# Kernel optimization log

Hardware: AMD Instinct MI355X
Metric: run time of the kernel (lower is better)

The kernel has to match this reference:

```python
import jax, jax.numpy as jnp
import numpy as np

B, N, C, T = 512, 62, 8, 64
K = 8          # topk
HEADS = 4
OUT = 128
EPS = 1e-5     # BatchNorm1d eps
NEG_SLOPE = 0.2  # GATConv leaky_relu slope


def _gat(x, W, a_src, a_dst, bias, src, dst, valid, num_nodes, concat):
    """PyG GATConv (eval mode, self-loops already in edge list)."""
    H, Co = a_src.shape[1], a_src.shape[2]
    xl = (x @ W.T).reshape(num_nodes, H, Co)          # [V,H,Co]
    al_src = jnp.sum(xl * a_src, axis=-1)             # [V,H]
    al_dst = jnp.sum(xl * a_dst, axis=-1)             # [V,H]
    alpha = jax.nn.leaky_relu(al_src[src] + al_dst[dst], NEG_SLOPE)  # [E,H]
    alpha = jnp.where(valid[:, None], alpha, -jnp.inf)
    amax = jax.ops.segment_max(alpha, dst, num_segments=num_nodes)   # [V,H]
    ex = jnp.where(valid[:, None], jnp.exp(alpha - amax[dst]), 0.0)
    denom = jax.ops.segment_sum(ex, dst, num_segments=num_nodes)     # [V,H]
    w = ex / denom[dst]                                              # softmax per dst
    out = jax.ops.segment_sum(xl[src] * w[:, :, None], dst, num_segments=num_nodes)
    out = out.reshape(num_nodes, H * Co) if concat else out.mean(axis=1)
    return out + bias


def reference(x, edge_index, W1, W2, b_sp, V_sp, bn_w, bn_b,
              g1_w, g1_asrc, g1_adst, g1_b, g2_w, g2_asrc, g2_adst, g2_b):
    # edge_index is unused: spatial=True rebuilds the graph from attention.
    x4 = x.reshape(B, N, C, T)
    # SpatialAttention: ((x @ W1) @ W2) -> tanh(. @ V + b) -> BatchNorm1d(N)
    prod = jnp.einsum('bnct,t->bnc', x4, W1) @ W2      # [B,N,N]
    S = jnp.tanh(prod @ V_sp + b_sp)                   # [B,N,N]
    mean = S.mean(axis=(0, 2), keepdims=True)          # BN over channel dim 1
    var = S.var(axis=(0, 2), keepdims=True)
    adj = (S - mean) / jnp.sqrt(var + EPS) * bn_w[None, :, None] + bn_b[None, :, None]
    # topk mask + dense_to_sparse: exactly K edges per (batch, row)
    _, idx = jax.lax.top_k(adj, K)                     # [B,N,K] column indices
    offs = (jnp.arange(B) * N)[:, None, None]
    src = (jnp.broadcast_to(jnp.arange(N)[None, :, None], (B, N, K)) + offs).reshape(-1)
    dst = (idx + offs).reshape(-1)
    # GATConv: remove_self_loops then add_self_loops -> mask topk self-edges, append loops
    loops = jnp.arange(B * N)
    valid = jnp.concatenate([src != dst, jnp.ones(B * N, dtype=bool)])
    src = jnp.concatenate([src, loops])
    dst = jnp.concatenate([dst, loops])
    h = x4.reshape(B * N, C * T)
    h = jax.nn.relu(_gat(h, g1_w, g1_asrc, g1_adst, g1_b, src, dst, valid, B * N, True))
    h = jax.nn.relu(_gat(h, g2_w, g2_asrc, g2_adst, g2_b, src, dst, valid, B * N, False))
    return h


def setup_inputs() -> dict:
    key = jax.random.key(0)
    ks = jax.random.split(key, 16)
    d_in = C * T  # 512
    return {
        'x': jax.random.normal(ks[0], (B, N, C, T), jnp.float32),
        'edge_index': jax.random.randint(ks[1], (2, 128), 0, B * N, jnp.int64) if False else jax.random.randint(ks[1], (2, 128), 0, B * N).astype(jnp.int32),
        'W1': jax.random.uniform(ks[2], (T,), jnp.float32),
        'W2': jax.random.normal(ks[3], (C, N), jnp.float32) * 0.1,
        'b_sp': jax.random.normal(ks[4], (1, N, N), jnp.float32) * 0.1,
        'V_sp': jax.random.normal(ks[5], (N, N), jnp.float32) * 0.1,
        'bn_w': jnp.ones((N,), jnp.float32),
        'bn_b': jnp.zeros((N,), jnp.float32),
        'g1_w': jax.random.normal(ks[6], (HEADS * OUT, d_in), jnp.float32) * 0.04,
        'g1_asrc': jax.random.normal(ks[7], (1, HEADS, OUT), jnp.float32) * 0.06,
        'g1_adst': jax.random.normal(ks[8], (1, HEADS, OUT), jnp.float32) * 0.06,
        'g1_b': jnp.zeros((HEADS * OUT,), jnp.float32),
        'g2_w': jax.random.normal(ks[9], (HEADS * OUT, HEADS * OUT), jnp.float32) * 0.04,
        'g2_asrc': jax.random.normal(ks[10], (1, HEADS, OUT), jnp.float32) * 0.06,
        'g2_adst': jax.random.normal(ks[11], (1, HEADS, OUT), jnp.float32) * 0.06,
        'g2_b': jnp.zeros((OUT,), jnp.float32),
    }
```

## Files before the change

### kernel.cpp

```cpp
#include <hip/hip_runtime.h>
#include <math.h>

#define B_ 512
#define N_ 62
#define V_ (B_ * N_)
#define MP_ (B_ * 64)
#define TOPK_ 8

typedef __attribute__((ext_vector_type(8))) short bf16x8;
typedef __attribute__((ext_vector_type(4))) float f32x4;

__device__ __forceinline__ unsigned short bf16rn(float f) {
    unsigned int u = __float_as_uint(f);
    unsigned int r = (u + 0x7fffu + ((u >> 16) & 1u)) >> 16;
    return (unsigned short)r;
}
__device__ __forceinline__ float bf16tof(unsigned short h) {
    return __uint_as_float(((unsigned int)h) << 16);
}

__device__ __forceinline__ void gload16(const void* g, void* l) {
    __builtin_amdgcn_global_load_lds(
        (const __attribute__((address_space(1))) unsigned int*)g,
        (__attribute__((address_space(3))) unsigned int*)l, 16, 0, 0);
}

__global__ __launch_bounds__(256) void spatial_S(
    const float* __restrict__ x, const float* __restrict__ W1,
    const float* __restrict__ W2, const float* __restrict__ bsp,
    const float* __restrict__ Vsp, float* __restrict__ S,
    unsigned short* __restrict__ A2)
{
    int w = threadIdx.x >> 6, lane = threadIdx.x & 63;
    int blk = blockIdx.x * 4 + w;
    int b = blk / N_, n = blk - b * N_;
    const float* xr = x + (size_t)blk * 512;
    float w1 = W1[lane];

    float y[8];
#pragma unroll
    for (int c = 0; c < 8; ++c) {
        float xv = xr[c * 64 + lane];
        A2[((size_t)(b * 64 + n)) * 512 + c * 64 + lane] = bf16rn(xv);
        float p = xv * w1;
#pragma unroll
        for (int off = 32; off; off >>= 1) p += __shfl_xor(p, off);
        y[c] = p;
    }

    __shared__ float pr[4][N_];
    if (lane < N_) {
        float acc = 0.f;
#pragma unroll
        for (int c = 0; c < 8; ++c) acc += y[c] * W2[c * N_ + lane];
        pr[w][lane] = acc;
    }
    __syncthreads();
    if (lane < N_) {
        float acc = bsp[n * N_ + lane];
        for (int k = 0; k < N_; ++k) acc += pr[w][k] * Vsp[k * N_ + lane];
        S[(size_t)blk * N_ + lane] = tanhf(acc);
    }
}

__global__ __launch_bounds__(256) void bn_part(
    const float* __restrict__ S, double* __restrict__ part)
{
    int n = blockIdx.x >> 4, slice = blockIdx.x & 15;
    double s = 0.0, s2 = 0.0;
    int i0 = slice * 1984;
    for (int i = i0 + threadIdx.x; i < i0 + 1984; i += 256) {
        int b = i / N_, m = i - b * N_;
        float v = S[((size_t)b * N_ + n) * N_ + m];
        s += v; s2 += (double)v * v;
    }
    __shared__ double sh[256], sh2[256];
    sh[threadIdx.x] = s; sh2[threadIdx.x] = s2;
    __syncthreads();
    for (int off = 128; off; off >>= 1) {
        if (threadIdx.x < off) {
            sh[threadIdx.x] += sh[threadIdx.x + off];
            sh2[threadIdx.x] += sh2[threadIdx.x + off];
        }
        __syncthreads();
    }
    if (threadIdx.x == 0) {
        part[((size_t)n * 16 + slice) * 2 + 0] = sh[0];
        part[((size_t)n * 16 + slice) * 2 + 1] = sh2[0];
    }
}

__global__ __launch_bounds__(64) void bn_final(
    const double* __restrict__ part, const float* __restrict__ bnw,
    const float* __restrict__ bnb, float* __restrict__ scale,
    float* __restrict__ shift)
{
    int n = threadIdx.x;
    if (n >= N_) return;
    double s = 0.0, s2 = 0.0;
    for (int j = 0; j < 16; ++j) {
        s  += part[((size_t)n * 16 + j) * 2 + 0];
        s2 += part[((size_t)n * 16 + j) * 2 + 1];
    }
    const double cnt = (double)(B_ * N_);
    double mean = s / cnt;
    double var = s2 / cnt - mean * mean;
    float inv = (float)(1.0 / sqrt(var + 1e-5));
    scale[n] = bnw[n] * inv;
    shift[n] = bnb[n] - (float)mean * bnw[n] * inv;
}

__global__ __launch_bounds__(64) void topk_mask(
    const float* __restrict__ S, const float* __restrict__ scale,
    const float* __restrict__ shift, unsigned long long* __restrict__ maskT)
{
    int blk = blockIdx.x;
    int b = blk / N_, n = blk - b * N_;
    int lane = threadIdx.x;
    float v = (lane < N_) ? S[(size_t)blk * N_ + lane] * scale[n] + shift[n]
                          : -INFINITY;
    bool sel = false;
#pragma unroll
    for (int k = 0; k < TOPK_; ++k) {
        float mv = v; int mi = lane;
#pragma unroll
        for (int off = 32; off; off >>= 1) {
            float ov = __shfl_xor(mv, off);
            int   oi = __shfl_xor(mi, off);
            if (ov > mv || (ov == mv && oi < mi)) { mv = ov; mi = oi; }
        }
        if (lane == mi) { sel = true; v = -INFINITY; }
    }
    unsigned long long row = __ballot(sel) | (1ull << n);
    if (lane < N_ && ((row >> lane) & 1ull))
        atomicOr(&maskT[(size_t)b * N_ + lane], 1ull << n);
}

__global__ __launch_bounds__(256) void zero_u64(unsigned long long* p, int n)
{
    int i = blockIdx.x * 256 + threadIdx.x;
    if (i < n) p[i] = 0ull;
}

__global__ __launch_bounds__(256) void split_pair(
    const float* __restrict__ in, unsigned short* __restrict__ out, int total4)
{
    int gid = blockIdx.x * 256 + threadIdx.x;
    if (gid >= total4) return;
    int row = gid >> 7;
    int c = (gid & 127) * 4;
    float4 v = ((const float4*)in)[gid];
    ushort4 h, l;
    float f;
    h.x = bf16rn(v.x); f = v.x - bf16tof(h.x); l.x = bf16rn(f);
    h.y = bf16rn(v.y); f = v.y - bf16tof(h.y); l.y = bf16rn(f);
    h.z = bf16rn(v.z); f = v.z - bf16tof(h.z); l.z = bf16rn(f);
    h.w = bf16rn(v.w); f = v.w - bf16tof(h.w); l.w = bf16rn(f);
    *(ushort4*)(&out[(size_t)row * 1024 + c])       = h;
    *(ushort4*)(&out[(size_t)row * 1024 + 512 + c]) = l;
}

__global__ __launch_bounds__(256) void gemm_bf16(
    const unsigned short* __restrict__ Ah, const unsigned short* __restrict__ Bw,
    unsigned short* __restrict__ XT,
    const float* __restrict__ asrc, const float* __restrict__ adst,
    float* __restrict__ als, float* __restrict__ ald)
{
    __shared__ __align__(16) unsigned short smem[16384];
    char* As = (char*)smem;
    char* Bs = (char*)(smem + 8192);

    int tid = threadIdx.x;
    int lane = tid & 63, w = tid >> 6;

    int flat = blockIdx.y * 4 + blockIdx.x;
    int swz = (flat & 7) * 128 + (flat >> 3);
    int by = swz >> 2, bx = swz & 3;
    int bm = by * 128, bn = bx * 128;

    int wr = w >> 1, wc = w & 1;

    f32x4 acc[4][4];
#pragma unroll
    for (int mf = 0; mf < 4; ++mf)
#pragma unroll
        for (int nf = 0; nf < 4; ++nf) acc[mf][nf] = (f32x4){0.f, 0.f, 0.f, 0.f};

    int srow = w * 8 + (lane >> 3);
    int kcol = (lane & 7) ^ (lane >> 3);
    int ldsoff = w * 1024;

    for (int kt = 0; kt < 16; ++kt) {
        int k0 = (kt & 7) * 64;
        int bBase = (kt >> 3) * 512 + k0;
#pragma unroll
        for (int i = 0; i < 4; ++i) {
            int row = i * 32 + srow;
            gload16(Ah + (size_t)(bm + row) * 512 + k0 + kcol * 8,
                    As + i * 4096 + ldsoff);
            gload16(Bw + (size_t)(bn + row) * 1024 + bBase + kcol * 8,
                    Bs + i * 4096 + ldsoff);
        }
        __syncthreads();

#pragma unroll
        for (int kk = 0; kk < 2; ++kk) {
            bf16x8 af[4], bfr[4];
#pragma unroll
            for (int mf = 0; mf < 4; ++mf)
                af[mf] = *(const bf16x8*)(As + (wr*64 + mf*16 + (lane&15))*128
                                             + ((kk*4 + (lane>>4)) ^ (lane&7))*16);
#pragma unroll
            for (int nf = 0; nf < 4; ++nf)
                bfr[nf] = *(const bf16x8*)(Bs + (wc*64 + nf*16 + (lane&15))*128
                                              + ((kk*4 + (lane>>4)) ^ (lane&7))*16);
#pragma unroll
            for (int mf = 0; mf < 4; ++mf)
#pragma unroll
                for (int nf = 0; nf < 4; ++nf)
                    acc[mf][nf] = __builtin_amdgcn_mfma_f32_16x16x32_bf16(
                        af[mf], bfr[nf], acc[mf][nf], 0, 0, 0);
        }
        __syncthreads();
    }

    int cc = lane & 15, lh = lane >> 4;
    int bb = (bm >> 6) + wr;
    int c0 = bn + wc * 64 + cc;
    int hH = bn >> 7;
    float as4[4], ad4[4];
#pragma unroll
    for (int nf = 0; nf < 4; ++nf) {
        as4[nf] = asrc[c0 + nf * 16];
        ad4[nf] = adst[c0 + nf * 16];
    }

#pragma unroll
    for (int mf = 0; mf < 4; ++mf) {
        int s = lh * 4 + mf * 16;
        f32x4 ts = (f32x4){0.f, 0.f, 0.f, 0.f};
        f32x4 td = (f32x4){0.f, 0.f, 0.f, 0.f};
#pragma unroll
        for (int nf = 0; nf < 4; ++nf) {
            ushort4 hv, lv;
#pragma unroll
            for (int r = 0; r < 4; ++r) {
                float v = acc[mf][nf][r];
                unsigned short hb = bf16rn(v);
                ((unsigned short*)&hv)[r] = hb;
                ((unsigned short*)&lv)[r] = bf16rn(v - bf16tof(hb));
                ts[r] += v * as4[nf];
                td[r] += v * ad4[nf];
            }
            size_t cb = ((size_t)bb * 1024 + c0 + nf * 16) * 64 + s;
            *(ushort4*)(XT + cb) = hv;
            *(ushort4*)(XT + cb + (size_t)512 * 64) = lv;
        }
#pragma unroll
        for (int off = 1; off < 16; off <<= 1) {
#pragma unroll
            for (int r = 0; r < 4; ++r) {
                ts[r] += __shfl_xor(ts[r], off);
                td[r] += __shfl_xor(td[r], off);
            }
        }
        if (cc == 0) {
#pragma unroll
            for (int r = 0; r < 4; ++r) {
                atomicAdd(&als[((size_t)bb * 64 + s + r) * 4 + hH], ts[r]);
                atomicAdd(&ald[((size_t)bb * 64 + s + r) * 4 + hH], td[r]);
            }
        }
    }
}

template <int APPLY>
__global__ __launch_bounds__(512, 8) void gat_aggM(
    const unsigned short* __restrict__ XT,
    const float* __restrict__ als, const float* __restrict__ ald,
    const unsigned long long* __restrict__ maskT,
    const float* __restrict__ bias,
    void* __restrict__ outp)
{
    __shared__ __align__(16) char lds[34816];
    float* shs = (float*)(lds + 32768);
    float* shd = (float*)(lds + 33792);

    int b = blockIdx.x;
    int tid = threadIdx.x;
    int lane = tid & 63, w = tid >> 6;

    if (tid < 256) {
        shs[tid] = als[(size_t)b * 256 + tid];
        shd[tid] = ald[(size_t)b * 256 + tid];
    }
    __syncthreads();

    for (int t = w; t < 248; t += 8) {
        int d = t >> 2, h = t & 3;
        unsigned long long m = maskT[(size_t)b * N_ + d];
        bool valid = (lane < N_) && ((m >> lane) & 1ull);
        float a = -INFINITY;
        if (valid) {
            float raw = shs[lane * 4 + h] + shd[d * 4 + h];
            a = (raw > 0.f) ? raw : 0.2f * raw;
        }
        float mx = a;
#pragma unroll
        for (int off = 32; off; off >>= 1) mx = fmaxf(mx, __shfl_xor(mx, off));
        float ex = valid ? expf(a - mx) : 0.f;
        float sm = ex;
#pragma unroll
        for (int off = 32; off; off >>= 1) sm += __shfl_xor(sm, off);
        float wv = valid ? ex / sm : 0.f;
        int addr = h * 8192 + d * 128
                 + (((lane >> 3) ^ (d & 7)) << 4) + ((lane & 7) << 1);
        *(unsigned short*)(lds + addr) = bf16rn(wv);
    }
    __syncthreads();

    int cc = lane & 15, lh = lane >> 4;
    const unsigned short* xb = XT + (size_t)b * 1024 * 64;

    union U16 { uint4 u; bf16x8 v; };

    f32x4 acc[4];
#pragma unroll
    for (int mf = 0; mf < 4; ++mf) acc[mf] = (f32x4){0.f, 0.f, 0.f, 0.f};

#pragma unroll
    for (int ch = 0; ch < 4; ++ch) {
        if (APPLY == 1 && ch > 0) {
#pragma unroll
            for (int mf = 0; mf < 4; ++mf) acc[mf] = (f32x4){0.f, 0.f, 0.f, 0.f};
        }

        const unsigned short* xp = xb + ((size_t)(ch * 128 + w * 16 + cc)) * 64
                                      + lh * 8;
#pragma unroll
        for (int kk = 0; kk < 2; ++kk) {
            U16 bh, bl;
            bh.u = *(const uint4*)(xp + kk * 32);
            bl.u = *(const uint4*)(xp + kk * 32 + (size_t)512 * 64);
            bf16x8 af[4];
#pragma unroll
            for (int mf = 0; mf < 4; ++mf)
                af[mf] = *(const bf16x8*)(lds + ch * 8192
                              + (mf * 16 + cc) * 128
                              + (((kk * 4 + lh) ^ (cc & 7)) << 4));
#pragma unroll
            for (int mf = 0; mf < 4; ++mf) {
                acc[mf] = __builtin_amdgcn_mfma_f32_16x16x32_bf16(
                    af[mf], bh.v, acc[mf], 0, 0, 0);
                acc[mf] = __builtin_amdgcn_mfma_f32_16x16x32_bf16(
                    af[mf], bl.v, acc[mf], 0, 0, 0);
            }
        }

        if (APPLY == 1) {
            int c = ch * 128 + w * 16 + cc;
            float bc = bias[c];
            unsigned short* H = (unsigned short*)outp;
#pragma unroll
            for (int mf = 0; mf < 4; ++mf)
#pragma unroll
                for (int r = 0; r < 4; ++r) {
                    int d = mf * 16 + lh * 4 + r;
                    if (d < N_) {
                        float v = acc[mf][r] + bc;
                        v = v > 0.f ? v : 0.f;
                        H[((size_t)b * 64 + d) * 512 + c] = bf16rn(v);
                    }
                }
        }
    }

    if (APPLY == 0) {
        int c = w * 16 + cc;
        float bc = bias[c];
        float* outF = (float*)outp;
#pragma unroll
        for (int mf = 0; mf < 4; ++mf)
#pragma unroll
            for (int r = 0; r < 4; ++r) {
                int d = mf * 16 + lh * 4 + r;
                if (d < N_) {
                    float v = acc[mf][r] * 0.25f + bc;
                    outF[((size_t)b * N_ + d) * 128 + c] = v > 0.f ? v : 0.f;
                }
            }
    }
}

extern "C" void kernel_launch(void* const* d_in, const int* in_sizes, int n_in,
                              void* d_out, int out_size, void* d_ws, size_t ws_size,
                              hipStream_t stream)
{
    const float* x    = (const float*)d_in[0];
    const float* W1   = (const float*)d_in[2];
    const float* W2   = (const float*)d_in[3];
    const float* bsp  = (const float*)d_in[4];
    const float* Vsp  = (const float*)d_in[5];
    const float* bnw  = (const float*)d_in[6];
    const float* bnb  = (const float*)d_in[7];
    const float* g1w  = (const float*)d_in[8];
    const float* g1as = (const float*)d_in[9];
    const float* g1ad = (const float*)d_in[10];
    const float* g1b  = (const float*)d_in[11];
    const float* g2w  = (const float*)d_in[12];
    const float* g2as = (const float*)d_in[13];
    const float* g2ad = (const float*)d_in[14];
    const float* g2b  = (const float*)d_in[15];
    float* out = (float*)d_out;

    char* ws = (char*)d_ws;
    size_t off = 0;
    auto alloc = [&](size_t bytes) -> void* {
        void* p = ws + off;
        off += (bytes + 255) & ~(size_t)255;
        return p;
    };
    float* S      = (float*)alloc((size_t)V_ * N_ * 4);
    float* scale  = (float*)alloc(N_ * 4);
    float* shift  = (float*)alloc(N_ * 4);
    double* part  = (double*)alloc((size_t)N_ * 16 * 2 * 8);
    unsigned long long* maskT = (unsigned long long*)alloc((size_t)V_ * 8);
    float* als    = (float*)alloc((size_t)MP_ * 4 * 4);
    float* ald    = (float*)alloc((size_t)MP_ * 4 * 4);
    unsigned short* A2  = (unsigned short*)alloc((size_t)MP_ * 512 * 2);
    unsigned short* Bw1 = (unsigned short*)alloc((size_t)512 * 1024 * 2);
    unsigned short* Bw2 = (unsigned short*)alloc((size_t)512 * 1024 * 2);
    unsigned short* XT  = (unsigned short*)alloc((size_t)B_ * 1024 * 64 * 2 + 256);
    unsigned short* H1  = (unsigned short*)alloc((size_t)MP_ * 512 * 2);

    zero_u64<<<(V_ + 255) / 256, 256, 0, stream>>>(maskT, V_);
    zero_u64<<<(MP_ * 4 * 2 / 2 + 255) / 256, 256, 0, stream>>>(
        (unsigned long long*)als, MP_ * 4 * 2 / 2);

    spatial_S<<<V_ / 4, 256, 0, stream>>>(x, W1, W2, bsp, Vsp, S, A2);
    bn_part<<<N_ * 16, 256, 0, stream>>>(S, part);
    bn_final<<<1, 64, 0, stream>>>(part, bnw, bnb, scale, shift);
    topk_mask<<<V_, 64, 0, stream>>>(S, scale, shift, maskT);

    split_pair<<<(512 * 128 + 255) / 256, 256, 0, stream>>>(g1w, Bw1, 512 * 128);
    split_pair<<<(512 * 128 + 255) / 256, 256, 0, stream>>>(g2w, Bw2, 512 * 128);

    dim3 gg(4, 256);
    gemm_bf16<<<gg, 256, 0, stream>>>(A2, Bw1, XT, g1as, g1ad, als, ald);
    gat_aggM<1><<<B_, 512, 0, stream>>>(XT, als, ald, maskT, g1b, H1);

    zero_u64<<<(MP_ * 4 * 2 / 2 + 255) / 256, 256, 0, stream>>>(
        (unsigned long long*)als, MP_ * 4 * 2 / 2);
    gemm_bf16<<<gg, 256, 0, stream>>>(H1, Bw2, XT, g2as, g2ad, als, ald);
    gat_aggM<0><<<B_, 512, 0, stream>>>(XT, als, ald, maskT, g2b, out);
}
```

Measured before the change: 446.9 us.

## Drop bf16 hi/lo split for XT and stage transposed stores through LDS

Stores the GEMM output XT as a single bf16 value instead of a hi+lo bf16 pair, which halves the XT buffer and removes the second MFMA and load per step in the aggregation kernel. The GEMM epilogue now writes the tile into swizzled shared memory and then emits coalesced 16-byte global stores, replacing scattered 8-byte stores. This lowers precision of the node features feeding aggregation, and adds a sync plus LDS reuse in the epilogue.

Measured after the change: 413.4 us. 7.5% less time.

```diff
diff --git a/kernel.cpp b/kernel.cpp
--- a/kernel.cpp
+++ b/kernel.cpp
@@ -226,35 +226,34 @@
 
     int cc = lane & 15, lh = lane >> 4;
     int bb = (bm >> 6) + wr;
-    int c0 = bn + wc * 64 + cc;
+    int c0 = bn + wc * 64;
     int hH = bn >> 7;
     float as4[4], ad4[4];
 #pragma unroll
     for (int nf = 0; nf < 4; ++nf) {
-        as4[nf] = asrc[c0 + nf * 16];
-        ad4[nf] = adst[c0 + nf * 16];
-    }
+        as4[nf] = asrc[c0 + nf * 16 + cc];
+        ad4[nf] = adst[c0 + nf * 16 + cc];
+    }
+
+    char* Wb = (char*)smem + w * 8192;
 
 #pragma unroll
     for (int mf = 0; mf < 4; ++mf) {
-        int s = lh * 4 + mf * 16;
         f32x4 ts = (f32x4){0.f, 0.f, 0.f, 0.f};
         f32x4 td = (f32x4){0.f, 0.f, 0.f, 0.f};
+        int t = mf * 4 + lh;
 #pragma unroll
         for (int nf = 0; nf < 4; ++nf) {
-            ushort4 hv, lv;
+            ushort4 hv;
 #pragma unroll
             for (int r = 0; r < 4; ++r) {
                 float v = acc[mf][nf][r];
-                unsigned short hb = bf16rn(v);
-                ((unsigned short*)&hv)[r] = hb;
-                ((unsigned short*)&lv)[r] = bf16rn(v - bf16tof(hb));
+                ((unsigned short*)&hv)[r] = bf16rn(v);
                 ts[r] += v * as4[nf];
                 td[r] += v * ad4[nf];
             }
-            size_t cb = ((size_t)bb * 1024 + c0 + nf * 16) * 64 + s;
-            *(ushort4*)(XT + cb) = hv;
-            *(ushort4*)(XT + cb + (size_t)512 * 64) = lv;
+            int c = nf * 16 + cc;
+            *(ushort4*)(Wb + c * 128 + ((t ^ (c & 15)) << 3)) = hv;
         }
 #pragma unroll
         for (int off = 1; off < 16; off <<= 1) {
@@ -265,11 +264,30 @@
             }
         }
         if (cc == 0) {
+            int s = lh * 4 + mf * 16;
 #pragma unroll
             for (int r = 0; r < 4; ++r) {
                 atomicAdd(&als[((size_t)bb * 64 + s + r) * 4 + hH], ts[r]);
                 atomicAdd(&ald[((size_t)bb * 64 + s + r) * 4 + hH], td[r]);
             }
+        }
+    }
+    __syncthreads();
+
+    {
+        int c = lane, m = c & 15;
+        const char* row = Wb + c * 128;
+        unsigned short* gp = XT + ((size_t)bb * 512 + c0 + c) * 64;
+#pragma unroll
+        for (int k = 0; k < 8; ++k) {
+            unsigned long long q0 =
+                *(const unsigned long long*)(row + (((2 * k) ^ m) << 3));
+            unsigned long long q1 =
+                *(const unsigned long long*)(row + (((2 * k + 1) ^ m) << 3));
+            uint4 o;
+            o.x = (unsigned int)q0; o.y = (unsigned int)(q0 >> 32);
+            o.z = (unsigned int)q1; o.w = (unsigned int)(q1 >> 32);
+            *(uint4*)(gp + k * 8) = o;
         }
     }
 }
@@ -320,7 +338,7 @@
     __syncthreads();
 
     int cc = lane & 15, lh = lane >> 4;
-    const unsigned short* xb = XT + (size_t)b * 1024 * 64;
+    const unsigned short* xb = XT + (size_t)b * 512 * 64;
 
     union U16 { uint4 u; bf16x8 v; };
 
@@ -339,9 +357,8 @@
                                       + lh * 8;
 #pragma unroll
         for (int kk = 0; kk < 2; ++kk) {
-            U16 bh, bl;
+            U16 bh;
             bh.u = *(const uint4*)(xp + kk * 32);
-            bl.u = *(const uint4*)(xp + kk * 32 + (size_t)512 * 64);
             bf16x8 af[4];
 #pragma unroll
             for (int mf = 0; mf < 4; ++mf)
@@ -349,12 +366,9 @@
                               + (mf * 16 + cc) * 128
                               + (((kk * 4 + lh) ^ (cc & 7)) << 4));
 #pragma unroll
-            for (int mf = 0; mf < 4; ++mf) {
+            for (int mf = 0; mf < 4; ++mf)
                 acc[mf] = __builtin_amdgcn_mfma_f32_16x16x32_bf16(
                     af[mf], bh.v, acc[mf], 0, 0, 0);
-                acc[mf] = __builtin_amdgcn_mfma_f32_16x16x32_bf16(
-                    af[mf], bl.v, acc[mf], 0, 0, 0);
-            }
         }
 
         if (APPLY == 1) {
@@ -430,7 +444,7 @@
     unsigned short* A2  = (unsigned short*)alloc((size_t)MP_ * 512 * 2);
     unsigned short* Bw1 = (unsigned short*)alloc((size_t)512 * 1024 * 2);
     unsigned short* Bw2 = (unsigned short*)alloc((size_t)512 * 1024 * 2);
-    unsigned short* XT  = (unsigned short*)alloc((size_t)B_ * 1024 * 64 * 2 + 256);
+    unsigned short* XT  = (unsigned short*)alloc((size_t)B_ * 512 * 64 * 2 + 256);
     unsigned short* H1  = (unsigned short*)alloc((size_t)MP_ * 512 * 2);
 
     zero_u64<<<(V_ + 255) / 256, 256, 0, stream>>>(maskT, V_);
```
